# Kernel tuning notes

Measured on AMD Instinct MI355X. Metric: run time of the kernel, lower is better.

Reference implementation:

```python
import jax, jax.numpy as jnp
import numpy as np

EPS_LN = 1e-5


def layer_norm(x, g, b):
    mu = jnp.mean(x, axis=-1, keepdims=True)
    var = jnp.mean((x - mu) ** 2, axis=-1, keepdims=True)
    return (x - mu) * jax.lax.rsqrt(var + EPS_LN) * g + b


def setup_inputs() -> dict:
    key = jax.random.key(0)
    ks = jax.random.split(key, 16)
    N, E, H, EA = 25000, 400000, 128, 1
    h = jax.random.normal(ks[0], (N, H), dtype=jnp.float32)
    coord = jax.random.normal(ks[1], (N, 3), dtype=jnp.float32)
    edge_index = jax.random.randint(ks[2], (2, E), 0, N, dtype=jnp.int64)
    edge_attr = jax.random.normal(ks[3], (E, EA), dtype=jnp.float32)

    def lin(k, fan_in, fan_out):
        lim = 1.0 / np.sqrt(fan_in)
        return jax.random.uniform(k, (fan_in, fan_out), jnp.float32, -lim, lim)

    in_edge = 2 * H + 1 + EA  # 258
    params = {
        'e_W1': lin(ks[4], in_edge, H), 'e_b1': jnp.zeros((H,), jnp.float32),
        'e_g1': jnp.ones((H,), jnp.float32), 'e_be1': jnp.zeros((H,), jnp.float32),
        'e_W2': lin(ks[5], H, H), 'e_b2': jnp.zeros((H,), jnp.float32),
        'e_g2': jnp.ones((H,), jnp.float32), 'e_be2': jnp.zeros((H,), jnp.float32),
        'n_W1': lin(ks[6], 2 * H, H), 'n_b1': jnp.zeros((H,), jnp.float32),
        'n_g1': jnp.ones((H,), jnp.float32), 'n_be1': jnp.zeros((H,), jnp.float32),
        'n_W2': lin(ks[7], H, H), 'n_b2': jnp.zeros((H,), jnp.float32),
        'c_W1': lin(ks[8], H, H), 'c_b1': jnp.zeros((H,), jnp.float32),
        'c_g1': jnp.ones((H,), jnp.float32), 'c_be1': jnp.zeros((H,), jnp.float32),
        # xavier_uniform with gain=0.001, no bias
        'c_W2': jax.random.uniform(ks[9], (H, 1), jnp.float32, -1.0, 1.0) * (0.001 * np.sqrt(6.0 / (H + 1))),
    }
    return dict(h=h, edge_index=edge_index, coord=coord, edge_attr=edge_attr, **params)


def reference(h, edge_index, coord, edge_attr,
              e_W1, e_b1, e_g1, e_be1, e_W2, e_b2, e_g2, e_be2,
              n_W1, n_b1, n_g1, n_be1, n_W2, n_b2,
              c_W1, c_b1, c_g1, c_be1, c_W2):
    N = h.shape[0]
    row, col = edge_index[0], edge_index[1]

    coord_diff = coord[row] - coord[col]                     # [E,3]
    radial = jnp.sum(coord_diff ** 2, axis=1, keepdims=True)  # [E,1]
    norm = jnp.sqrt(radial + 1e-8)
    coord_diff = coord_diff / (norm + 1.0)

    inp = jnp.concatenate([h[row], h[col], radial, edge_attr], axis=1)  # [E,258]
    x = jax.nn.silu(layer_norm(inp @ e_W1 + e_b1, e_g1, e_be1))
    edge_feat = jax.nn.silu(layer_norm(x @ e_W2 + e_b2, e_g2, e_be2))   # [E,H]

    cm = jax.nn.silu(layer_norm(edge_feat @ c_W1 + c_b1, c_g1, c_be1)) @ c_W2  # [E,1]
    trans = coord_diff * cm                                   # [E,3]

    coord_out = coord + jax.ops.segment_sum(trans, row, num_segments=N)
    agg = jax.ops.segment_sum(edge_feat, row, num_segments=N)  # [N,H]

    node_in = jnp.concatenate([h, agg], axis=1)               # [N,2H]
    out = jax.nn.silu(layer_norm(node_in @ n_W1 + n_b1, n_g1, n_be1)) @ n_W2 + n_b2
    out = h + out  # recurrent
    return out, coord_out
```

## Files before the change

kernel.cpp:

```cpp
#include <hip/hip_runtime.h>
#include <math.h>

#define H 128
#define KE 256
#define KN 256
#define XSTR 136
#define SSTR 132

typedef __attribute__((ext_vector_type(8))) short bf16x8;
typedef __attribute__((ext_vector_type(4))) float f32x4;

__device__ __forceinline__ float silu_f(float x) { return x / (1.0f + __expf(-x)); }

__device__ __forceinline__ unsigned short f2bf(float f) {
    unsigned int u = __float_as_uint(f);
    unsigned int r = u + 0x7FFFu + ((u >> 16) & 1u);
    return (unsigned short)(r >> 16);
}

__device__ __forceinline__ unsigned int pkbf(float a, float b) {
#if defined(__has_builtin)
#if __has_builtin(__builtin_amdgcn_cvt_pk_bf16_f32)
    typedef __attribute__((ext_vector_type(2))) __bf16 bf16x2_t;
    bf16x2_t v = __builtin_amdgcn_cvt_pk_bf16_f32(a, b);
    return *(unsigned int*)&v;
#else
    return (unsigned int)f2bf(a) | ((unsigned int)f2bf(b) << 16);
#endif
#else
    return (unsigned int)f2bf(a) | ((unsigned int)f2bf(b) << 16);
#endif
}

__device__ __forceinline__ float bflo(unsigned int w) { return __uint_as_float(w << 16); }
__device__ __forceinline__ float bfhi(unsigned int w) { return __uint_as_float(w & 0xFFFF0000u); }

__device__ __forceinline__ void atomic_pk_add_bf16(unsigned short* addr, unsigned int pkv) {
    asm volatile("global_atomic_pk_add_bf16 %0, %1, off"
                 :: "v"(addr), "v"(pkv) : "memory");
}

template<int CTRL>
__device__ __forceinline__ float dpp_add(float x) {
    int t = __builtin_amdgcn_update_dpp(0, __float_as_int(x), CTRL, 0xF, 0xF, true);
    return x + __int_as_float(t);
}
__device__ __forceinline__ float red16(float x) {
    x = dpp_add<0x128>(x);
    x = dpp_add<0x124>(x);
    x = dpp_add<0x122>(x);
    x = dpp_add<0x121>(x);
    return x;
}

__device__ __forceinline__ void wfrag(const float* __restrict__ W,
                                      unsigned short* __restrict__ Wf, int f) {
    int kb = f >> 9, rem = f & 511;
    int nt = rem >> 6, lane = rem & 63;
    int quad = lane >> 4, l15 = lane & 15;
    int n = nt * 16 + l15, k0 = kb * 32 + quad * 8;
    union { bf16x8 v; unsigned short u[8]; } pk;
    #pragma unroll
    for (int j = 0; j < 8; ++j) pk.u[j] = f2bf(W[(size_t)(k0 + j) * H + n]);
    *(bf16x8*)&Wf[(size_t)f * 8] = pk.v;
}

__global__ __launch_bounds__(256) void prep_all(
    const float* __restrict__ h, unsigned short* __restrict__ hb, int n4_h,
    float* __restrict__ aggz, int n4_agg,
    const float* __restrict__ coord, float* __restrict__ coord_out, int n_coord,
    const float* __restrict__ eW1, const float* __restrict__ eW2,
    const float* __restrict__ cW1, const float* __restrict__ nW1,
    const float* __restrict__ nW2,
    unsigned short* __restrict__ eW1f, unsigned short* __restrict__ eW2f,
    unsigned short* __restrict__ cW1f, unsigned short* __restrict__ nW1f,
    unsigned short* __restrict__ nW2f,
    int b0, int b1, int b2)
{
    int b = blockIdx.x;
    int t = threadIdx.x;
    if (b < b0) {
        int i = b * 256 + t;
        if (i < n4_h) {
            float4 f = ((const float4*)h)[i];
            ((uint2*)hb)[i] = make_uint2(pkbf(f.x, f.y), pkbf(f.z, f.w));
        }
    } else if (b < b1) {
        int i = (b - b0) * 256 + t;
        if (i < n4_agg) ((float4*)aggz)[i] = (float4){0.f, 0.f, 0.f, 0.f};
    } else if (b < b2) {
        int i = (b - b1) * 256 + t;
        if (i < n_coord) coord_out[i] = coord[i];
    } else {
        int idx = (b - b2) * 256 + t;
        if      (idx <  4096) wfrag(eW1, eW1f, idx);
        else if (idx <  8192) wfrag(nW1, nW1f, idx - 4096);
        else if (idx < 10240) wfrag(eW2, eW2f, idx - 8192);
        else if (idx < 12288) wfrag(cW1, cW1f, idx - 10240);
        else if (idx < 14336) wfrag(nW2, nW2f, idx - 12288);
    }
}

__global__ __launch_bounds__(256, 4) void proj_kernel(
    const unsigned short* __restrict__ hb,
    const unsigned short* __restrict__ eW1f,
    unsigned short* __restrict__ Pb, int N)
{
    __shared__ unsigned short Ys[4][16 * 256];

    const int wv = threadIdx.x >> 6;
    const int lane = threadIdx.x & 63;
    const int l15 = lane & 15, quad = lane >> 4;
    const int gn0 = (blockIdx.x * 4 + wv) * 16;
    unsigned short* Y = &Ys[wv][0];

    if (gn0 >= N) return;
    int nl = gn0 + l15; if (nl >= N) nl = N - 1;

    f32x4 a1[8], a2[8];
    #pragma unroll
    for (int nt = 0; nt < 8; ++nt) {
        a1[nt] = (f32x4){0.f, 0.f, 0.f, 0.f};
        a2[nt] = (f32x4){0.f, 0.f, 0.f, 0.f};
    }

    for (int kb = 0; kb < 4; ++kb) {
        int ko = kb * 32 + quad * 8;
        bf16x8 af = *(const bf16x8*)(hb + (size_t)nl * H + ko);
        const unsigned short* bp1 = eW1f + ((size_t)kb * 8) * 512 + (size_t)lane * 8;
        const unsigned short* bp2 = eW1f + ((size_t)(kb + 4) * 8) * 512 + (size_t)lane * 8;
        #pragma unroll
        for (int nt = 0; nt < 8; ++nt) {
            bf16x8 b1 = *(const bf16x8*)(bp1 + (size_t)nt * 512);
            bf16x8 b2 = *(const bf16x8*)(bp2 + (size_t)nt * 512);
            a1[nt] = __builtin_amdgcn_mfma_f32_16x16x32_bf16(af, b1, a1[nt], 0, 0, 0);
            a2[nt] = __builtin_amdgcn_mfma_f32_16x16x32_bf16(af, b2, a2[nt], 0, 0, 0);
        }
    }

    #pragma unroll
    for (int nt = 0; nt < 8; ++nt) {
        int c = nt * 16 + l15;
        #pragma unroll
        for (int r = 0; r < 4; ++r) {
            int rr = quad * 4 + r;
            Y[rr * 256 + c]       = f2bf(a1[nt][r]);
            Y[rr * 256 + 128 + c] = f2bf(a2[nt][r]);
        }
    }

    const int m = lane >> 2, part = lane & 3;
    int gm = gn0 + m; if (gm >= N) gm = N - 1;
    #pragma unroll
    for (int j = 0; j < 8; ++j) {
        uint4 v = *(const uint4*)&Y[m * 256 + part * 64 + j * 8];
        *(uint4*)(Pb + (size_t)gm * 256 + part * 64 + j * 8) = v;
    }
}

__device__ __forceinline__ void ln_silu_store1(
    f32x4* acc, const float* __restrict__ bias, const float* __restrict__ g,
    const float* __restrict__ be, unsigned short* X, int l15, int quad)
{
    float s[4] = {0,0,0,0}, q[4] = {0,0,0,0};
    #pragma unroll
    for (int nt = 0; nt < 8; ++nt) {
        float b = bias[nt * 16 + l15];
        #pragma unroll
        for (int r = 0; r < 4; ++r) {
            float x = acc[nt][r] + b; acc[nt][r] = x; s[r] += x; q[r] += x * x;
        }
    }
    #pragma unroll
    for (int r = 0; r < 4; ++r) { s[r] = red16(s[r]); q[r] = red16(q[r]); }
    #pragma unroll
    for (int r = 0; r < 4; ++r) {
        float mu = s[r] * 0.0078125f, v = q[r] * 0.0078125f - mu * mu;
        s[r] = mu; q[r] = rsqrtf(v + 1e-5f);
    }
    #pragma unroll
    for (int nt = 0; nt < 8; ++nt) {
        float gg = g[nt * 16 + l15], bb = be[nt * 16 + l15];
        #pragma unroll
        for (int r = 0; r < 4; ++r) {
            float a = q[r] * gg, c = bb - s[r] * a;
            float y = silu_f(fmaf(acc[nt][r], a, c));
            acc[nt][r] = y;
            X[(quad * 4 + r) * XSTR + nt * 16 + l15] = f2bf(y);
        }
    }
}

__global__ __launch_bounds__(64, 4) void edge_kernel(
    const unsigned short* __restrict__ Pb, const int* __restrict__ ei,
    const float* __restrict__ coord, const float* __restrict__ eattr,
    const float* __restrict__ eW1,
    const float* __restrict__ eb1, const float* __restrict__ eg1, const float* __restrict__ ebe1,
    const unsigned short* __restrict__ eW2f,
    const float* __restrict__ eb2, const float* __restrict__ eg2, const float* __restrict__ ebe2,
    const unsigned short* __restrict__ cW1f,
    const float* __restrict__ cb1, const float* __restrict__ cg1, const float* __restrict__ cbe1,
    const float* __restrict__ cW2,
    unsigned short* __restrict__ aggb, float* __restrict__ coord_out, int E)
{
    __shared__ float S[16 * SSTR];
    unsigned short* X = (unsigned short*)S;

    const int lane = threadIdx.x;
    const int l15 = lane & 15, quad = lane >> 4;
    const int ge0 = blockIdx.x * 16;

    int el  = ge0 + l15;
    int elc = (el < E) ? el : (E - 1);
    int rowl = ei[elc], coll = ei[E + elc];
    float dx = coord[rowl * 3 + 0] - coord[coll * 3 + 0];
    float dy = coord[rowl * 3 + 1] - coord[coll * 3 + 1];
    float dz = coord[rowl * 3 + 2] - coord[coll * 3 + 2];
    float radial = dx * dx + dy * dy + dz * dz;
    float inv = 1.0f / (sqrtf(radial + 1e-8f) + 1.0f);
    float cdx = dx * inv, cdy = dy * inv, cdz = dz * inv;
    float ea = eattr[elc];

    {
        const int m = lane >> 2, part = lane & 3;
        int row_m = __shfl(rowl, m, 64);
        int col_m = __shfl(coll, m, 64);
        const unsigned short* p1 = Pb + (size_t)row_m * 256 + part * 32;
        const unsigned short* p2 = Pb + (size_t)col_m * 256 + 128 + part * 32;
        #pragma unroll
        for (int j = 0; j < 4; ++j) {
            uint4 a = *(const uint4*)(p1 + j * 8);
            uint4 b = *(const uint4*)(p2 + j * 8);
            float4 v0, v1;
            v0.x = bflo(a.x) + bflo(b.x); v0.y = bfhi(a.x) + bfhi(b.x);
            v0.z = bflo(a.y) + bflo(b.y); v0.w = bfhi(a.y) + bfhi(b.y);
            v1.x = bflo(a.z) + bflo(b.z); v1.y = bfhi(a.z) + bfhi(b.z);
            v1.z = bflo(a.w) + bflo(b.w); v1.w = bfhi(a.w) + bfhi(b.w);
            *(float4*)&S[m * SSTR + part * 32 + j * 8]     = v0;
            *(float4*)&S[m * SSTR + part * 32 + j * 8 + 4] = v1;
        }
    }

    f32x4 acc[8];
    {
        float rad_r[4], ea_r[4];
        #pragma unroll
        for (int r = 0; r < 4; ++r) {
            rad_r[r] = __shfl(radial, quad * 4 + r, 64);
            ea_r[r]  = __shfl(ea,     quad * 4 + r, 64);
        }
        #pragma unroll
        for (int nt = 0; nt < 8; ++nt) {
            float w256 = eW1[256 * H + nt * 16 + l15];
            float w257 = eW1[257 * H + nt * 16 + l15];
            #pragma unroll
            for (int r = 0; r < 4; ++r) {
                float base = S[(quad * 4 + r) * SSTR + nt * 16 + l15];
                acc[nt][r] = base + rad_r[r] * w256 + ea_r[r] * w257;
            }
        }
    }

    ln_silu_store1(acc, eb1, eg1, ebe1, X, l15, quad);

    f32x4 ac2[8];
    #pragma unroll
    for (int nt = 0; nt < 8; ++nt) ac2[nt] = (f32x4){0.f, 0.f, 0.f, 0.f};
    for (int kb = 0; kb < 4; ++kb) {
        bf16x8 af = *(const bf16x8*)&X[l15 * XSTR + kb * 32 + quad * 8];
        const unsigned short* bp = eW2f + ((size_t)kb * 8) * 512 + (size_t)lane * 8;
        #pragma unroll
        for (int nt = 0; nt < 8; ++nt) {
            bf16x8 bf = *(const bf16x8*)(bp + (size_t)nt * 512);
            ac2[nt] = __builtin_amdgcn_mfma_f32_16x16x32_bf16(af, bf, ac2[nt], 0, 0, 0);
        }
    }

    ln_silu_store1(ac2, eb2, eg2, ebe2, X, l15, quad);

    {
        int rowm[4];
        #pragma unroll
        for (int r = 0; r < 4; ++r) rowm[r] = __shfl(rowl, quad * 4 + r, 64);
        #pragma unroll
        for (int c4 = 0; c4 < 4; ++c4) {
            #pragma unroll
            for (int r = 0; r < 4; ++r) {
                int geh = ge0 + quad * 4 + r;
                if (geh < E) {
                    unsigned int pkv =
                        *(const unsigned int*)&X[(quad * 4 + r) * XSTR + c4 * 32 + 2 * l15];
                    atomic_pk_add_bf16(aggb + (size_t)rowm[r] * H + c4 * 32 + 2 * l15, pkv);
                }
            }
        }
    }

    #pragma unroll
    for (int nt = 0; nt < 8; ++nt) acc[nt] = (f32x4){0.f, 0.f, 0.f, 0.f};
    for (int kb = 0; kb < 4; ++kb) {
        bf16x8 af = *(const bf16x8*)&X[l15 * XSTR + kb * 32 + quad * 8];
        const unsigned short* bp = cW1f + ((size_t)kb * 8) * 512 + (size_t)lane * 8;
        #pragma unroll
        for (int nt = 0; nt < 8; ++nt) {
            bf16x8 bf = *(const bf16x8*)(bp + (size_t)nt * 512);
            acc[nt] = __builtin_amdgcn_mfma_f32_16x16x32_bf16(af, bf, acc[nt], 0, 0, 0);
        }
    }

    {
        float s[4] = {0,0,0,0}, q[4] = {0,0,0,0};
        #pragma unroll
        for (int nt = 0; nt < 8; ++nt) {
            float b = cb1[nt * 16 + l15];
            #pragma unroll
            for (int r = 0; r < 4; ++r) {
                float x = acc[nt][r] + b; acc[nt][r] = x; s[r] += x; q[r] += x * x;
            }
        }
        #pragma unroll
        for (int r = 0; r < 4; ++r) { s[r] = red16(s[r]); q[r] = red16(q[r]); }
        #pragma unroll
        for (int r = 0; r < 4; ++r) {
            float mu = s[r] * 0.0078125f, v = q[r] * 0.0078125f - mu * mu;
            s[r] = mu; q[r] = rsqrtf(v + 1e-5f);
        }
        float cm[4] = {0,0,0,0};
        #pragma unroll
        for (int nt = 0; nt < 8; ++nt) {
            float gg = cg1[nt * 16 + l15], bb = cbe1[nt * 16 + l15];
            float w2 = cW2[nt * 16 + l15];
            #pragma unroll
            for (int r = 0; r < 4; ++r) {
                float a = q[r] * gg, c = bb - s[r] * a;
                cm[r] += silu_f(fmaf(acc[nt][r], a, c)) * w2;
            }
        }
        #pragma unroll
        for (int r = 0; r < 4; ++r) cm[r] = red16(cm[r]);
        #pragma unroll
        for (int r = 0; r < 4; ++r) {
            int src = quad * 4 + r;
            float cdxr = __shfl(cdx, src, 64);
            float cdyr = __shfl(cdy, src, 64);
            float cdzr = __shfl(cdz, src, 64);
            int rw = __shfl(rowl, src, 64);
            float comp = (l15 == 0) ? cdxr : ((l15 == 1) ? cdyr : cdzr);
            int geh = ge0 + src;
            if (l15 < 3 && geh < E)
                atomicAdd(&coord_out[(size_t)rw * 3 + l15], comp * cm[r]);
        }
    }
}

__global__ __launch_bounds__(256, 4) void node_kernel(
    const unsigned short* __restrict__ hb, const float* __restrict__ h,
    const unsigned short* __restrict__ aggb,
    const unsigned short* __restrict__ nW1f,
    const float* __restrict__ nb1, const float* __restrict__ ng1, const float* __restrict__ nbe1,
    const unsigned short* __restrict__ nW2f, const float* __restrict__ nb2,
    float* __restrict__ out, int N)
{
    __shared__ unsigned short Xs[4][16 * XSTR];

    const int wv   = threadIdx.x >> 6;
    const int lane = threadIdx.x & 63;
    const int l15 = lane & 15, quad = lane >> 4;
    const int gn0 = (blockIdx.x * 4 + wv) * 16;
    unsigned short* X = &Xs[wv][0];

    if (gn0 >= N) return;
    int nl = gn0 + l15; if (nl >= N) nl = N - 1;

    f32x4 acc[8];
    #pragma unroll
    for (int nt = 0; nt < 8; ++nt) acc[nt] = (f32x4){0.f, 0.f, 0.f, 0.f};

    for (int kb = 0; kb < 8; ++kb) {
        int ko = (kb & 3) * 32 + quad * 8;
        const unsigned short* src = (kb < 4) ? hb : aggb;
        bf16x8 af = *(const bf16x8*)(src + (size_t)nl * H + ko);
        const unsigned short* bp = nW1f + ((size_t)kb * 8) * 512 + (size_t)lane * 8;
        #pragma unroll
        for (int nt = 0; nt < 8; ++nt) {
            bf16x8 bf = *(const bf16x8*)(bp + (size_t)nt * 512);
            acc[nt] = __builtin_amdgcn_mfma_f32_16x16x32_bf16(af, bf, acc[nt], 0, 0, 0);
        }
    }

    ln_silu_store1(acc, nb1, ng1, nbe1, X, l15, quad);

    f32x4 ac2[8];
    #pragma unroll
    for (int nt = 0; nt < 8; ++nt) ac2[nt] = (f32x4){0.f, 0.f, 0.f, 0.f};
    for (int kb = 0; kb < 4; ++kb) {
        bf16x8 af = *(const bf16x8*)&X[l15 * XSTR + kb * 32 + quad * 8];
        const unsigned short* bp = nW2f + ((size_t)kb * 8) * 512 + (size_t)lane * 8;
        #pragma unroll
        for (int nt = 0; nt < 8; ++nt) {
            bf16x8 bf = *(const bf16x8*)(bp + (size_t)nt * 512);
            ac2[nt] = __builtin_amdgcn_mfma_f32_16x16x32_bf16(af, bf, ac2[nt], 0, 0, 0);
        }
    }

    #pragma unroll
    for (int nt = 0; nt < 8; ++nt) {
        float b = nb2[nt * 16 + l15];
        #pragma unroll
        for (int r = 0; r < 4; ++r) {
            int gn = gn0 + quad * 4 + r;
            if (gn < N) {
                size_t idx = (size_t)gn * H + nt * 16 + l15;
                out[idx] = ac2[nt][r] + b + h[idx];
            }
        }
    }
}

extern "C" void kernel_launch(void* const* d_in, const int* in_sizes, int n_in,
                              void* d_out, int out_size, void* d_ws, size_t ws_size,
                              hipStream_t stream) {
    const float* h     = (const float*)d_in[0];
    const int*   ei    = (const int*)d_in[1];
    const float* coord = (const float*)d_in[2];
    const float* eattr = (const float*)d_in[3];
    const float* eW1   = (const float*)d_in[4];
    const float* eb1   = (const float*)d_in[5];
    const float* eg1   = (const float*)d_in[6];
    const float* ebe1  = (const float*)d_in[7];
    const float* eW2   = (const float*)d_in[8];
    const float* eb2   = (const float*)d_in[9];
    const float* eg2   = (const float*)d_in[10];
    const float* ebe2  = (const float*)d_in[11];
    const float* nW1   = (const float*)d_in[12];
    const float* nb1   = (const float*)d_in[13];
    const float* ng1   = (const float*)d_in[14];
    const float* nbe1  = (const float*)d_in[15];
    const float* nW2   = (const float*)d_in[16];
    const float* nb2   = (const float*)d_in[17];
    const float* cW1   = (const float*)d_in[18];
    const float* cb1   = (const float*)d_in[19];
    const float* cg1   = (const float*)d_in[20];
    const float* cbe1  = (const float*)d_in[21];
    const float* cW2   = (const float*)d_in[22];

    const int N = in_sizes[0] / H;
    const int E = in_sizes[1] / 2;

    float* out       = (float*)d_out;
    float* coord_out = out + (size_t)N * H;

    char* ws = (char*)d_ws;
    size_t o = 0;
    unsigned short* aggb = (unsigned short*)(ws + o); o += (size_t)N * H * 2;
    unsigned short* hb   = (unsigned short*)(ws + o); o += (size_t)N * H * 2;
    unsigned short* Pb   = (unsigned short*)(ws + o); o += (size_t)N * 256 * 2;
    unsigned short* eW1f = (unsigned short*)(ws + o); o += (size_t)H * KE * 2;
    unsigned short* eW2f = (unsigned short*)(ws + o); o += (size_t)H * H * 2;
    unsigned short* cW1f = (unsigned short*)(ws + o); o += (size_t)H * H * 2;
    unsigned short* nW1f = (unsigned short*)(ws + o); o += (size_t)H * KN * 2;
    unsigned short* nW2f = (unsigned short*)(ws + o); o += (size_t)H * H * 2;

    const int n4_h   = N * H / 4;
    const int n4_agg = N * H / 8;
    const int n_co   = N * 3;
    const int b0 = (n4_h   + 255) / 256;
    const int b1 = b0 + (n4_agg + 255) / 256;
    const int b2 = b1 + (n_co   + 255) / 256;
    const int bw = (4096 + 4096 + 2048 + 2048 + 2048 + 255) / 256;
    prep_all<<<b2 + bw, 256, 0, stream>>>(
        h, hb, n4_h, (float*)aggb, n4_agg, coord, coord_out, n_co,
        eW1, eW2, cW1, nW1, nW2,
        eW1f, eW2f, cW1f, nW1f, nW2f, b0, b1, b2);

    proj_kernel<<<(N + 63) / 64, 256, 0, stream>>>(hb, eW1f, Pb, N);

    edge_kernel<<<(E + 15) / 16, 64, 0, stream>>>(
        Pb, ei, coord, eattr,
        eW1, eb1, eg1, ebe1,
        eW2f, eb2, eg2, ebe2,
        cW1f, cb1, cg1, cbe1, cW2,
        aggb, coord_out, E);

    node_kernel<<<(N + 63) / 64, 256, 0, stream>>>(
        hb, h, aggb, nW1f, nb1, ng1, nbe1, nW2f, nb2, out, N);
}
```

Before: 322.4 us.

## Fuse first edge layer-norm into gather, pack four waves per block, fast math

The first edge layer (gather of the projected row/col features, radial and edge-attr terms, bias, LayerNorm, SiLU) is now computed directly in registers by the lanes that load each edge row. The result is written once as bf16 to LDS, replacing the fp32 staging buffer and its transposed re-read. The edge kernel now runs four independent 16-edge waves per 256-thread block with a higher occupancy hint. Reciprocal, rsqrt and sqrt use the AMDGCN fast intrinsics. This removes an LDS round trip and raises waves per block, at the cost of a 32-float register array per lane and slightly less precise math.

```diff
diff --git a/kernel.cpp b/kernel.cpp
--- a/kernel.cpp
+++ b/kernel.cpp
@@ -5,12 +5,35 @@
 #define KE 256
 #define KN 256
 #define XSTR 136
-#define SSTR 132
 
 typedef __attribute__((ext_vector_type(8))) short bf16x8;
 typedef __attribute__((ext_vector_type(4))) float f32x4;
 
-__device__ __forceinline__ float silu_f(float x) { return x / (1.0f + __expf(-x)); }
+__device__ __forceinline__ float fast_rcp(float x) {
+#if defined(__has_builtin) && __has_builtin(__builtin_amdgcn_rcpf)
+    return __builtin_amdgcn_rcpf(x);
+#else
+    return 1.0f / x;
+#endif
+}
+__device__ __forceinline__ float fast_rsq(float x) {
+#if defined(__has_builtin) && __has_builtin(__builtin_amdgcn_rsqf)
+    return __builtin_amdgcn_rsqf(x);
+#else
+    return rsqrtf(x);
+#endif
+}
+__device__ __forceinline__ float fast_sqrt(float x) {
+#if defined(__has_builtin) && __has_builtin(__builtin_amdgcn_sqrtf)
+    return __builtin_amdgcn_sqrtf(x);
+#else
+    return sqrtf(x);
+#endif
+}
+
+__device__ __forceinline__ float silu_f(float x) {
+    return x * fast_rcp(1.0f + __expf(-x));
+}
 
 __device__ __forceinline__ unsigned short f2bf(float f) {
     unsigned int u = __float_as_uint(f);
@@ -176,7 +199,7 @@
     #pragma unroll
     for (int r = 0; r < 4; ++r) {
         float mu = s[r] * 0.0078125f, v = q[r] * 0.0078125f - mu * mu;
-        s[r] = mu; q[r] = rsqrtf(v + 1e-5f);
+        s[r] = mu; q[r] = fast_rsq(v + 1e-5f);
     }
     #pragma unroll
     for (int nt = 0; nt < 8; ++nt) {
@@ -191,7 +214,7 @@
     }
 }
 
-__global__ __launch_bounds__(64, 4) void edge_kernel(
+__global__ __launch_bounds__(256, 6) void edge_kernel(
     const unsigned short* __restrict__ Pb, const int* __restrict__ ei,
     const float* __restrict__ coord, const float* __restrict__ eattr,
     const float* __restrict__ eW1,
@@ -203,12 +226,15 @@
     const float* __restrict__ cW2,
     unsigned short* __restrict__ aggb, float* __restrict__ coord_out, int E)
 {
-    __shared__ float S[16 * SSTR];
-    unsigned short* X = (unsigned short*)S;
-
-    const int lane = threadIdx.x;
+    __shared__ unsigned short Xs[4][16 * XSTR];
+
+    const int wv   = threadIdx.x >> 6;
+    const int lane = threadIdx.x & 63;
     const int l15 = lane & 15, quad = lane >> 4;
-    const int ge0 = blockIdx.x * 16;
+    const int ge0 = (blockIdx.x * 4 + wv) * 16;
+    unsigned short* X = &Xs[wv][0];
+
+    if (ge0 >= E) return;
 
     int el  = ge0 + l15;
     int elc = (el < E) ? el : (E - 1);
@@ -217,51 +243,75 @@
     float dy = coord[rowl * 3 + 1] - coord[coll * 3 + 1];
     float dz = coord[rowl * 3 + 2] - coord[coll * 3 + 2];
     float radial = dx * dx + dy * dy + dz * dz;
-    float inv = 1.0f / (sqrtf(radial + 1e-8f) + 1.0f);
+    float inv = fast_rcp(fast_sqrt(radial + 1e-8f) + 1.0f);
     float cdx = dx * inv, cdy = dy * inv, cdz = dz * inv;
     float ea = eattr[elc];
 
     {
         const int m = lane >> 2, part = lane & 3;
-        int row_m = __shfl(rowl, m, 64);
-        int col_m = __shfl(coll, m, 64);
+        int row_m   = __shfl(rowl,   m, 64);
+        int col_m   = __shfl(coll,   m, 64);
+        float rad_m = __shfl(radial, m, 64);
+        float ea_m  = __shfl(ea,     m, 64);
         const unsigned short* p1 = Pb + (size_t)row_m * 256 + part * 32;
         const unsigned short* p2 = Pb + (size_t)col_m * 256 + 128 + part * 32;
+        const float* w6 = eW1 + 256 * H + part * 32;
+        const float* w7 = eW1 + 257 * H + part * 32;
+        const float* bb = eb1 + part * 32;
+
+        float v[32];
+        float s = 0.f, q = 0.f;
         #pragma unroll
         for (int j = 0; j < 4; ++j) {
             uint4 a = *(const uint4*)(p1 + j * 8);
             uint4 b = *(const uint4*)(p2 + j * 8);
-            float4 v0, v1;
-            v0.x = bflo(a.x) + bflo(b.x); v0.y = bfhi(a.x) + bfhi(b.x);
-            v0.z = bflo(a.y) + bflo(b.y); v0.w = bfhi(a.y) + bfhi(b.y);
-            v1.x = bflo(a.z) + bflo(b.z); v1.y = bfhi(a.z) + bfhi(b.z);
-            v1.z = bflo(a.w) + bflo(b.w); v1.w = bfhi(a.w) + bfhi(b.w);
-            *(float4*)&S[m * SSTR + part * 32 + j * 8]     = v0;
-            *(float4*)&S[m * SSTR + part * 32 + j * 8 + 4] = v1;
-        }
-    }
-
-    f32x4 acc[8];
-    {
-        float rad_r[4], ea_r[4];
-        #pragma unroll
-        for (int r = 0; r < 4; ++r) {
-            rad_r[r] = __shfl(radial, quad * 4 + r, 64);
-            ea_r[r]  = __shfl(ea,     quad * 4 + r, 64);
-        }
-        #pragma unroll
-        for (int nt = 0; nt < 8; ++nt) {
-            float w256 = eW1[256 * H + nt * 16 + l15];
-            float w257 = eW1[257 * H + nt * 16 + l15];
+            float4 wA = *(const float4*)(w6 + j * 8);
+            float4 wB = *(const float4*)(w6 + j * 8 + 4);
+            float4 uA = *(const float4*)(w7 + j * 8);
+            float4 uB = *(const float4*)(w7 + j * 8 + 4);
+            float4 bA = *(const float4*)(bb + j * 8);
+            float4 bB = *(const float4*)(bb + j * 8 + 4);
+            float* vp = v + j * 8;
+            vp[0] = bflo(a.x) + bflo(b.x) + rad_m * wA.x + ea_m * uA.x + bA.x;
+            vp[1] = bfhi(a.x) + bfhi(b.x) + rad_m * wA.y + ea_m * uA.y + bA.y;
+            vp[2] = bflo(a.y) + bflo(b.y) + rad_m * wA.z + ea_m * uA.z + bA.z;
+            vp[3] = bfhi(a.y) + bfhi(b.y) + rad_m * wA.w + ea_m * uA.w + bA.w;
+            vp[4] = bflo(a.z) + bflo(b.z) + rad_m * wB.x + ea_m * uB.x + bB.x;
+            vp[5] = bfhi(a.z) + bfhi(b.z) + rad_m * wB.y + ea_m * uB.y + bB.y;
+            vp[6] = bflo(a.w) + bflo(b.w) + rad_m * wB.z + ea_m * uB.z + bB.z;
+            vp[7] = bfhi(a.w) + bfhi(b.w) + rad_m * wB.w + ea_m * uB.w + bB.w;
             #pragma unroll
-            for (int r = 0; r < 4; ++r) {
-                float base = S[(quad * 4 + r) * SSTR + nt * 16 + l15];
-                acc[nt][r] = base + rad_r[r] * w256 + ea_r[r] * w257;
-            }
-        }
-    }
-
-    ln_silu_store1(acc, eb1, eg1, ebe1, X, l15, quad);
+            for (int t = 0; t < 8; ++t) { s += vp[t]; q += vp[t] * vp[t]; }
+        }
+        s += __shfl_xor(s, 1, 64); s += __shfl_xor(s, 2, 64);
+        q += __shfl_xor(q, 1, 64); q += __shfl_xor(q, 2, 64);
+        float mu   = s * 0.0078125f;
+        float rstd = fast_rsq(q * 0.0078125f - mu * mu + 1e-5f);
+
+        const float* gg = eg1  + part * 32;
+        const float* be = ebe1 + part * 32;
+        unsigned short* Xrow = X + m * XSTR + part * 32;
+        #pragma unroll
+        for (int j = 0; j < 4; ++j) {
+            float4 gA = *(const float4*)(gg + j * 8);
+            float4 gB = *(const float4*)(gg + j * 8 + 4);
+            float4 eA = *(const float4*)(be + j * 8);
+            float4 eB = *(const float4*)(be + j * 8 + 4);
+            const float* vp = v + j * 8;
+            float y0 = silu_f(fmaf(vp[0] - mu, rstd * gA.x, eA.x));
+            float y1 = silu_f(fmaf(vp[1] - mu, rstd * gA.y, eA.y));
+            float y2 = silu_f(fmaf(vp[2] - mu, rstd * gA.z, eA.z));
+            float y3 = silu_f(fmaf(vp[3] - mu, rstd * gA.w, eA.w));
+            float y4 = silu_f(fmaf(vp[4] - mu, rstd * gB.x, eB.x));
+            float y5 = silu_f(fmaf(vp[5] - mu, rstd * gB.y, eB.y));
+            float y6 = silu_f(fmaf(vp[6] - mu, rstd * gB.z, eB.z));
+            float y7 = silu_f(fmaf(vp[7] - mu, rstd * gB.w, eB.w));
+            uint4 o;
+            o.x = pkbf(y0, y1); o.y = pkbf(y2, y3);
+            o.z = pkbf(y4, y5); o.w = pkbf(y6, y7);
+            *(uint4*)(Xrow + j * 8) = o;
+        }
+    }
 
     f32x4 ac2[8];
     #pragma unroll
@@ -296,6 +346,7 @@
         }
     }
 
+    f32x4 acc[8];
     #pragma unroll
     for (int nt = 0; nt < 8; ++nt) acc[nt] = (f32x4){0.f, 0.f, 0.f, 0.f};
     for (int kb = 0; kb < 4; ++kb) {
@@ -323,7 +374,7 @@
         #pragma unroll
         for (int r = 0; r < 4; ++r) {
             float mu = s[r] * 0.0078125f, v = q[r] * 0.0078125f - mu * mu;
-            s[r] = mu; q[r] = rsqrtf(v + 1e-5f);
+            s[r] = mu; q[r] = fast_rsq(v + 1e-5f);
         }
         float cm[4] = {0,0,0,0};
         #pragma unroll
@@ -475,7 +526,7 @@
 
     proj_kernel<<<(N + 63) / 64, 256, 0, stream>>>(hb, eW1f, Pb, N);
 
-    edge_kernel<<<(E + 15) / 16, 64, 0, stream>>>(
+    edge_kernel<<<(E + 63) / 64, 256, 0, stream>>>(
         Pb, ei, coord, eattr,
         eW1, eb1, eg1, ebe1,
         eW2f, eb2, eg2, ebe2,
```

Result: slower. 431.9 us (+34.0%).
